# Optimization experiments

Hardware: AMD Instinct MI355X
Metric: run time of the kernel (lower is better)

## Reference

```python
import jax, jax.numpy as jnp
import numpy as np

EPS = 1e-5  # BatchNorm eps
K_NEIGH = 32


def cdist(a, b):
    # a: (B,M,3), b: (B,N,3) -> (B,M,N) euclidean distances
    d2 = (jnp.sum(a * a, -1)[:, :, None] + jnp.sum(b * b, -1)[:, None, :]
          - 2.0 * jnp.einsum('bmd,bnd->bmn', a, b))
    return jnp.sqrt(jnp.maximum(d2, 0.0))


def bn(x, axes):
    # training-mode BatchNorm with gamma=1, beta=0 (fresh init); channel = remaining axis
    m = jnp.mean(x, axes, keepdims=True)
    v = jnp.var(x, axes, keepdims=True)
    return (x - m) / jnp.sqrt(v + EPS)


def gather_nb(x, idx):
    # x: (B,N,C), idx: (B,M,k) int -> (B,M,k,C)
    return jax.vmap(lambda xb, ib: xb[ib])(x, idx)


def sa_wslfa(xyz, feat, M, k, Wf, bf, Wa, ba):
    # xyz: (B,N,3), feat: (B,N,C) channel-last
    B, N, _ = xyz.shape
    idxc = jnp.linspace(0.0, N - 1, M).astype(jnp.int32)  # fps_uniform
    centers = xyz[:, idxc]                                 # (B,M,3)
    d = cdist(centers, xyz)                                # (B,M,N)
    _, idx_knn = jax.lax.top_k(-d, min(k, N))              # k smallest dists
    nx = gather_nb(xyz, idx_knn) - centers[:, :, None, :]  # local coords (B,M,k,3)
    nf = gather_nb(feat, idx_knn)                          # (B,M,k,C)
    cat = jnp.concatenate([nx, nf], -1)                    # (B,M,k,3+C)
    fp = jax.nn.relu(bn(jnp.einsum('bmkd,od->bmko', cat, Wf) + bf, (0, 1, 2)))
    ain = jnp.concatenate([cat, fp - jnp.mean(fp, 2, keepdims=True)], -1)
    alpha = jax.nn.relu(bn(jnp.einsum('bmkd,od->bmko', ain, Wa) + ba, (0, 1, 2)))
    w = jax.nn.softmax(alpha, axis=2)                      # softmax over k neighbors
    return centers, jnp.sum(w * fp, axis=2)                # (B,M,out)


def fp_layer(xyz_l, xyz_h, fl, fh, W, b):
    # 3-NN inverse-distance interpolation + 1x1 conv MLP
    d = cdist(xyz_l, xyz_h)
    kk = min(3, xyz_h.shape[1])
    negd, idx = jax.lax.top_k(-d, kk)
    d3 = jnp.maximum(-negd, 1e-8)
    w = 1.0 / d3
    w = w / jnp.sum(w, -1, keepdims=True)
    fi = jnp.sum(w[..., None] * gather_nb(fh, idx), 2)     # (B,Nl,Ch)
    x = jnp.concatenate([fi, fl], -1)
    return jax.nn.relu(bn(jnp.einsum('bnc,oc->bno', x, W) + b, (0, 1)))


def _forward(X, W_spfe1, b_spfe1, W_spfe2, b_spfe2, Wf1, bf1, Wa1, ba1,
             Wf2, bf2, Wa2, ba2, Wf3, bf3, Wa3, ba3,
             Wfp3, bfp3, Wfp2, bfp2, Wfp1, bfp1, Wh1, bh1, Wh2, bh2):
    B, N, C = X.shape
    xyz = X[:, :, :3]
    xyz_c = xyz - jnp.mean(xyz, 1, keepdims=True)
    normals = jnp.zeros_like(xyz)                          # C==3 path: zero normals
    spfe_in = jnp.concatenate([xyz, xyz_c, normals], -1)   # (B,N,9)
    h = jax.nn.relu(bn(jnp.einsum('bnd,od->bno', spfe_in, W_spfe1) + b_spfe1, (0, 1)))
    f0 = jax.nn.relu(bn(jnp.einsum('bnd,od->bno', h, W_spfe2) + b_spfe2, (0, 1)))
    M1, M2, M3 = max(1, N // 4), max(1, N // 8), max(1, N // 16)
    xyz1, f1 = sa_wslfa(xyz, f0, M1, K_NEIGH, Wf1, bf1, Wa1, ba1)
    xyz2, f2 = sa_wslfa(xyz1, f1, M2, K_NEIGH, Wf2, bf2, Wa2, ba2)
    xyz3, f3 = sa_wslfa(xyz2, f2, M3, K_NEIGH, Wf3, bf3, Wa3, ba3)
    f_up2 = fp_layer(xyz2, xyz3, f2, f3, Wfp3, bfp3)
    f_up1 = fp_layer(xyz1, xyz2, f1, f_up2, Wfp2, bfp2)
    f_up0 = fp_layer(xyz, xyz1, f0, f_up1, Wfp1, bfp1)
    hh = jax.nn.relu(bn(jnp.einsum('bnc,oc->bno', f_up0, Wh1) + bh1, (0, 1)))
    # dropout is identity in deterministic reference
    return jnp.einsum('bnc,oc->bno', hh, Wh2) + bh2        # (B,N,num_classes)


def setup_inputs() -> dict:
    key = jax.random.key(0)
    ks = jax.random.split(key, 32)

    def w(i, o, c):
        return jax.random.normal(ks[i], (o, c), jnp.float32) * (2.0 / c) ** 0.5

    def bias(i, o):
        return jax.random.normal(ks[i], (o,), jnp.float32) * 0.01

    return {
        'X': jax.random.normal(ks[0], (8, 4096, 3), jnp.float32),
        'W_spfe1': w(1, 64, 9), 'b_spfe1': bias(2, 64),
        'W_spfe2': w(3, 64, 64), 'b_spfe2': bias(4, 64),
        'Wf1': w(5, 128, 67), 'bf1': bias(6, 128),
        'Wa1': w(7, 128, 195), 'ba1': bias(8, 128),
        'Wf2': w(9, 256, 131), 'bf2': bias(10, 256),
        'Wa2': w(11, 256, 387), 'ba2': bias(12, 256),
        'Wf3': w(13, 512, 259), 'bf3': bias(14, 512),
        'Wa3': w(15, 512, 771), 'ba3': bias(16, 512),
        'Wfp3': w(17, 256, 768), 'bfp3': bias(18, 256),
        'Wfp2': w(19, 128, 384), 'bfp2': bias(20, 128),
        'Wfp1': w(21, 128, 192), 'bfp1': bias(22, 128),
        'Wh1': w(23, 128, 128), 'bh1': bias(24, 128),
        'Wh2': w(25, 50, 128), 'bh2': bias(26, 50),
    }


def reference(X, W_spfe1, b_spfe1, W_spfe2, b_spfe2, Wf1, bf1, Wa1, ba1,
              Wf2, bf2, Wa2, ba2, Wf3, bf3, Wa3, ba3,
              Wfp3, bfp3, Wfp2, bfp2, Wfp1, bfp1, Wh1, bh1, Wh2, bh2):
    return _forward(X, W_spfe1, b_spfe1, W_spfe2, b_spfe2, Wf1, bf1, Wa1, ba1,
                    Wf2, bf2, Wa2, ba2, Wf3, bf3, Wa3, ba3,
                    Wfp3, bfp3, Wfp2, bfp2, Wfp1, bfp1, Wh1, bh1, Wh2, bh2)
```

## Files before the change

kernel.cpp:

```cpp
#include <hip/hip_runtime.h>
#include <hip/hip_bf16.h>
#include <cstdint>
#include <cstddef>

#define KN 32
#define EPSV 1e-5f
#define BR 64
#define BO 64
#define BKK 16
#define ASTR 68
#define BKM 32
#define BKP 40

typedef float f32x4 __attribute__((ext_vector_type(4)));
typedef __bf16 bf16x8 __attribute__((ext_vector_type(8)));
typedef unsigned short ushort8 __attribute__((ext_vector_type(8)));

static inline int ceil_div(int a, int b) { return (a + b - 1) / b; }

__device__ __forceinline__ float b2f(unsigned short u) {
  union { float f; uint32_t i; } x;
  x.i = (uint32_t)u << 16;
  return x.f;
}

__global__ void convw_kernel(const float* W, __hip_bfloat16* Wb, int wk, int colOff,
                             long long tot, int K) {
  long long i = (long long)blockIdx.x * blockDim.x + threadIdx.x;
  if (i >= tot) return;
  int o = (int)(i / K), c = (int)(i % K);
  Wb[i] = __float2bfloat16(W[(size_t)o * wk + colOff + c]);
}

struct MdArgs {
  const float* Af; const unsigned short* Ab; int lda;
  const float* W; int wk; int colOff;
  const unsigned short* Wb;
  float* outf; __hip_bfloat16* outb;
  float* partial; int numOt;
  const unsigned short* Ga; const float* Gm;
  const float* xyz; const float* ctr; const int* idx;
  int M, Ncur;
  int R, K, O;
};

template <int EP, bool ABF16, bool WBF16>
__global__ __launch_bounds__(256) void gemm_mdw(MdArgs g) {
  __shared__ __align__(16) char smemraw[(128 + 64) * BKP * 2];
  __shared__ float nxs[128][3];
  __shared__ float waxs[64][3];
  __shared__ int grow[128];
  __hip_bfloat16* As = (__hip_bfloat16*)smemraw;
  __hip_bfloat16* Ws = As + 128 * BKP;
  const int tid = threadIdx.x;
  const int lane = tid & 63, w = tid >> 6;
  const int cpx = gridDim.x >> 3;
  const int s = (blockIdx.x & 7) * cpx + (blockIdx.x >> 3);
  const int rt = s / g.numOt;
  const int ot = s - rt * g.numOt;
  const int br0 = rt * 128, bo0 = ot * BO;

  if constexpr (EP == 2) {
    if (tid < 128) {
      int r = br0 + tid;
      int bm = r >> 5;
      int b = bm / g.M;
      int n = g.idx[(size_t)bm * KN + (r & (KN - 1))];
      int nb = b * g.Ncur + n;
      grow[tid] = nb;
      nxs[tid][0] = g.xyz[(size_t)nb * 3 + 0] - g.ctr[(size_t)bm * 3 + 0];
      nxs[tid][1] = g.xyz[(size_t)nb * 3 + 1] - g.ctr[(size_t)bm * 3 + 1];
      nxs[tid][2] = g.xyz[(size_t)nb * 3 + 2] - g.ctr[(size_t)bm * 3 + 2];
    } else if (tid < 192) {
      int o = tid - 128;
      waxs[o][0] = g.W[(size_t)(bo0 + o) * g.wk + 0];
      waxs[o][1] = g.W[(size_t)(bo0 + o) * g.wk + 1];
      waxs[o][2] = g.W[(size_t)(bo0 + o) * g.wk + 2];
    }
  }

  f32x4 acc[2][4] = {};
  const int arow0 = (w * 16 + (lane & 15)) * BKP + (lane >> 4) * 8;
  const int arow1 = arow0 + 64 * BKP;
  const int wr = tid >> 2;
  const int wkb = (tid & 3) * 8;
  const float* wrow = WBF16 ? nullptr : (g.W + (size_t)(bo0 + wr) * g.wk + g.colOff);

  for (int k0 = 0; k0 < g.K; k0 += BKM) {
#pragma unroll
    for (int p = 0; p < 2; ++p) {
      int i = tid + p * 256;
      int r = i >> 2, c8 = (i & 3) * 8;
      if constexpr (ABF16) {
        ushort8 v = *(const ushort8*)(g.Ab + (size_t)(br0 + r) * g.lda + k0 + c8);
        *(ushort8*)((unsigned short*)As + r * BKP + c8) = v;
      } else {
        const float* ap = g.Af + (size_t)(br0 + r) * g.lda + k0 + c8;
#pragma unroll
        for (int e = 0; e < 8; ++e) As[r * BKP + c8 + e] = __float2bfloat16(ap[e]);
      }
    }
    if constexpr (WBF16) {
      ushort8 v = *(const ushort8*)(g.Wb + (size_t)(bo0 + wr) * g.K + k0 + wkb);
      *(ushort8*)((unsigned short*)Ws + wr * BKP + wkb) = v;
    } else {
#pragma unroll
      for (int e = 0; e < 8; ++e)
        Ws[wr * BKP + wkb + e] = __float2bfloat16(wrow[k0 + wkb + e]);
    }
    __syncthreads();
    bf16x8 av0 = *(const bf16x8*)(As + arow0);
    bf16x8 av1 = *(const bf16x8*)(As + arow1);
#pragma unroll
    for (int nf = 0; nf < 4; ++nf) {
      bf16x8 bv = *(const bf16x8*)(Ws + (nf * 16 + (lane & 15)) * BKP + (lane >> 4) * 8);
      acc[0][nf] = __builtin_amdgcn_mfma_f32_16x16x32_bf16(av0, bv, acc[0][nf], 0, 0, 0);
      acc[1][nf] = __builtin_amdgcn_mfma_f32_16x16x32_bf16(av1, bv, acc[1][nf], 0, 0, 0);
    }
    __syncthreads();
  }

  const int col0 = lane & 15;
  float* red0 = (float*)smemraw;
  float* red1 = (float*)smemraw + 256;

#pragma unroll
  for (int rf = 0; rf < 2; ++rf) {
    const int rbase = rf * 64 + w * 16 + (lane >> 4) * 4;
    if constexpr (EP == 0) {
#pragma unroll
      for (int nf = 0; nf < 4; ++nf) {
        int o = bo0 + nf * 16 + col0;
#pragma unroll
        for (int e = 0; e < 4; ++e)
          g.outf[(size_t)(br0 + rbase + e) * g.O + o] = acc[rf][nf][e];
      }
    }
    if constexpr (EP == 1) {
#pragma unroll
      for (int nf = 0; nf < 4; ++nf) {
        int o = bo0 + nf * 16 + col0;
#pragma unroll
        for (int e = 0; e < 4; ++e)
          g.outb[(size_t)(br0 + rbase + e) * g.O + o] = __float2bfloat16(acc[rf][nf][e]);
      }
    }
    if constexpr (EP == 2 || EP == 3) {
      float vals[4][4];
#pragma unroll
      for (int nf = 0; nf < 4; ++nf) {
        int ol = nf * 16 + col0;
        int o = bo0 + ol;
#pragma unroll
        for (int e = 0; e < 4; ++e) {
          int rl = rbase + e;
          float v = acc[rf][nf][e];
          if constexpr (EP == 2) {
            int bmg = (br0 + rl) >> 5;
            v += b2f(g.Ga[(size_t)grow[rl] * g.O + o]) +
                 nxs[rl][0] * waxs[ol][0] + nxs[rl][1] * waxs[ol][1] +
                 nxs[rl][2] * waxs[ol][2] - g.Gm[(size_t)bmg * g.O + o];
          }
          vals[nf][e] = v;
          if constexpr (EP == 2)
            g.outb[(size_t)(br0 + rl) * g.O + o] = __float2bfloat16(v);
          else
            g.outf[(size_t)(br0 + rl) * g.O + o] = v;
        }
      }
#pragma unroll
      for (int nf = 0; nf < 4; ++nf) {
        float s0 = vals[nf][0] + vals[nf][1] + vals[nf][2] + vals[nf][3];
        float s1 = vals[nf][0] * vals[nf][0] + vals[nf][1] * vals[nf][1] +
                   vals[nf][2] * vals[nf][2] + vals[nf][3] * vals[nf][3];
        s0 += __shfl_xor(s0, 16); s0 += __shfl_xor(s0, 32);
        s1 += __shfl_xor(s1, 16); s1 += __shfl_xor(s1, 32);
        if ((lane >> 4) == 0) {
          red0[w * 64 + nf * 16 + lane] = s0;
          red1[w * 64 + nf * 16 + lane] = s1;
        }
      }
      __syncthreads();
      if (tid < 64) {
        float t0 = red0[tid] + red0[64 + tid] + red0[128 + tid] + red0[192 + tid];
        float t1 = red1[tid] + red1[64 + tid] + red1[128 + tid] + red1[192 + tid];
        size_t base = ((size_t)(rt * 2 + rf) * g.numOt + ot) * 128;
        g.partial[base + tid] = t0;
        g.partial[base + 64 + tid] = t1;
      }
      __syncthreads();
    }
  }
}

__global__ __launch_bounds__(256) void combine_fp_kernel(
    const unsigned short* Gf, const float* Wf, int wk,
    const float* xyz, const float* ctr, const int* idx,
    __hip_bfloat16* fpout, float* partial, int numOt, int M, int Ncur, int O) {
  __shared__ float tile[64][68];
  __shared__ float nxs[64][3];
  __shared__ float wfx[64][3];
  __shared__ int grow[64];
  int tid = threadIdx.x;
  int rt = blockIdx.x, ot = blockIdx.y;
  int br0 = rt * 64, bo0 = ot * 64;
  if (tid < 64) {
    int r = br0 + tid;
    int bm = r >> 5;
    int b = bm / M;
    int n = idx[(size_t)bm * KN + (r & (KN - 1))];
    int nb = b * Ncur + n;
    grow[tid] = nb;
    nxs[tid][0] = xyz[(size_t)nb * 3 + 0] - ctr[(size_t)bm * 3 + 0];
    nxs[tid][1] = xyz[(size_t)nb * 3 + 1] - ctr[(size_t)bm * 3 + 1];
    nxs[tid][2] = xyz[(size_t)nb * 3 + 2] - ctr[(size_t)bm * 3 + 2];
  } else if (tid < 128) {
    int o = tid - 64;
    wfx[o][0] = Wf[(size_t)(bo0 + o) * wk + 0];
    wfx[o][1] = Wf[(size_t)(bo0 + o) * wk + 1];
    wfx[o][2] = Wf[(size_t)(bo0 + o) * wk + 2];
  }
  __syncthreads();
  int rr = tid >> 2, os = (tid & 3) * 16;
  const unsigned short* gr = Gf + (size_t)grow[rr] * O + bo0 + os;
  ushort8 v0 = *(const ushort8*)gr;
  ushort8 v1 = *(const ushort8*)(gr + 8);
  __hip_bfloat16* outp = fpout + (size_t)(br0 + rr) * O + bo0 + os;
  float nx0 = nxs[rr][0], nx1 = nxs[rr][1], nx2 = nxs[rr][2];
#pragma unroll
  for (int i = 0; i < 16; ++i) {
    float gv = b2f(i < 8 ? v0[i] : v1[i - 8]);
    int o = os + i;
    float val = gv + nx0 * wfx[o][0] + nx1 * wfx[o][1] + nx2 * wfx[o][2];
    tile[rr][o] = val;
    outp[i] = __float2bfloat16(val);
  }
  __syncthreads();
  if (tid < 64) {
    float s = 0.f, s2 = 0.f;
#pragma unroll 4
    for (int r2 = 0; r2 < 64; ++r2) {
      float v = tile[r2][tid];
      s += v; s2 += v * v;
    }
    size_t base = ((size_t)rt * numOt + ot) * 128;
    partial[base + tid] = s;
    partial[base + 64 + tid] = s2;
  }
}

__global__ __launch_bounds__(64) void bn_fpmean_kernel(__hip_bfloat16* fp, const float2* stats2,
                                                       __hip_bfloat16* outm, int O) {
  int bm = blockIdx.x;
  int o = blockIdx.y * 64 + threadIdx.x;
  float2 st = stats2[o];
  __hip_bfloat16* p = fp + (size_t)bm * KN * O + o;
  float s = 0.f;
#pragma unroll
  for (int kk = 0; kk < KN; ++kk) {
    float v = __bfloat162float(p[(size_t)kk * O]);
    float y = fmaxf((v - st.x) * st.y, 0.f);
    __hip_bfloat16 yb = __float2bfloat16(y);
    p[(size_t)kk * O] = yb;
    s += __bfloat162float(yb);
  }
  outm[(size_t)bm * O + o] = __float2bfloat16(s * (1.f / KN));
}

__global__ __launch_bounds__(64) void apply_lite_kernel(const __hip_bfloat16* alpha,
                                                        const __hip_bfloat16* fp,
                                                        const float2* stats2, float* fout, int O) {
  int bm = blockIdx.x;
  int o = blockIdx.y * 64 + threadIdx.x;
  float2 st = stats2[o];
  size_t base = (size_t)bm * KN * O + o;
  float a[KN];
  float mx = -3.4e38f;
#pragma unroll
  for (int kk = 0; kk < KN; ++kk) {
    float v = fmaxf((__bfloat162float(alpha[base + (size_t)kk * O]) - st.x) * st.y, 0.f);
    a[kk] = v; mx = fmaxf(mx, v);
  }
  float s = 0.f;
#pragma unroll
  for (int kk = 0; kk < KN; ++kk) { float e = expf(a[kk] - mx); a[kk] = e; s += e; }
  float acc = 0.f;
#pragma unroll
  for (int kk = 0; kk < KN; ++kk) acc += a[kk] * __bfloat162float(fp[base + (size_t)kk * O]);
  fout[(size_t)bm * O + o] = acc / s;
}

struct GemmArgs {
  const float* A; const float* W; const float* bias;
  float* out; __hip_bfloat16* outb;
  float* partial; const float2* stats2; float* fout;
  const __hip_bfloat16* fpb; const float* fpmean;
  const float* xyz; const float* feat; const float* ctr; const int* idx; const float* bmean;
  int R, K, O, numOt, M, Cf, Of, Ncur;
};

template <int EMODE, int MODE>
__global__ __launch_bounds__(256) void gemm_dense(GemmArgs g) {
  __shared__ float smem[2 * BKK * ASTR];
  float* As = smem;
  float* Ws = smem + BKK * ASTR;
  const int tid = threadIdx.x;
  const int tr = tid >> 4, tc = tid & 15;
  const int rt = blockIdx.x, ot = blockIdx.y;
  const int br0 = rt * BR, bo0 = ot * BO;
  float acc[4][4] = {};
  for (int k0 = 0; k0 < g.K; k0 += BKK) {
    for (int i = tid; i < BR * BKK; i += 256) {
      int rr = i >> 4, cc = i & 15;
      int c = k0 + cc;
      float v = 0.f;
      if (c < g.K) {
        if constexpr (MODE == 0) {
          v = g.A[(size_t)(br0 + rr) * g.K + c];
        } else {
          int r = br0 + rr;
          int b = r / g.Ncur, n = r - b * g.Ncur;
          if (c < 3) v = g.xyz[((size_t)b * g.Ncur + n) * 3 + c];
          else if (c < 6) v = g.xyz[((size_t)b * g.Ncur + n) * 3 + (c - 3)] - g.bmean[b * 3 + (c - 3)];
        }
      }
      As[cc * ASTR + rr] = v;
    }
    for (int i = tid; i < BO * BKK; i += 256) {
      int oo = i >> 4, cc = i & 15;
      int o = bo0 + oo, c = k0 + cc;
      Ws[cc * ASTR + oo] = (o < g.O && c < g.K) ? g.W[(size_t)o * g.K + c] : 0.f;
    }
    __syncthreads();
#pragma unroll
    for (int kk = 0; kk < BKK; ++kk) {
      float a0[4], w0[4];
#pragma unroll
      for (int i = 0; i < 4; ++i) a0[i] = As[kk * ASTR + tr * 4 + i];
#pragma unroll
      for (int j = 0; j < 4; ++j) w0[j] = Ws[kk * ASTR + tc * 4 + j];
#pragma unroll
      for (int i = 0; i < 4; ++i)
#pragma unroll
        for (int j = 0; j < 4; ++j) acc[i][j] += a0[i] * w0[j];
    }
    __syncthreads();
  }
#pragma unroll
  for (int i = 0; i < 4; ++i) {
    int r = br0 + tr * 4 + i;
    if (r >= g.R) continue;
#pragma unroll
    for (int j = 0; j < 4; ++j) {
      int o = bo0 + tc * 4 + j;
      if (o >= g.O) continue;
      float v = acc[i][j];
      if (EMODE == 0 && g.bias) v += g.bias[o];
      g.out[(size_t)r * g.O + o] = v;
    }
  }
  if constexpr (EMODE == 1) {
    float* red0 = smem;
    float* red1 = smem + 1024;
#pragma unroll
    for (int j = 0; j < 4; ++j) {
      float s0 = 0.f, s1 = 0.f;
#pragma unroll
      for (int i = 0; i < 4; ++i) { float v = acc[i][j]; s0 += v; s1 += v * v; }
      red0[tr * 64 + tc * 4 + j] = s0;
      red1[tr * 64 + tc * 4 + j] = s1;
    }
    __syncthreads();
    for (int st = 8; st >= 1; st >>= 1) {
      if (tr < st) {
#pragma unroll
        for (int j = 0; j < 4; ++j) {
          int cix = tc * 4 + j;
          red0[tr * 64 + cix] += red0[(tr + st) * 64 + cix];
          red1[tr * 64 + cix] += red1[(tr + st) * 64 + cix];
        }
      }
      __syncthreads();
    }
    if (tr == 0) {
      size_t base = ((size_t)rt * g.numOt + ot) * 128;
#pragma unroll
      for (int j = 0; j < 4; ++j) {
        int cix = tc * 4 + j;
        g.partial[base + cix] = red0[cix];
        g.partial[base + 64 + cix] = red1[cix];
      }
    }
  }
}

__global__ void reduce_finalize_kernel(const float* partial, float2* stats2,
                                       int Rt, int numOt, int R, int O) {
  int o = blockIdx.x;
  int ot = o >> 6, oo = o & 63;
  int tid = threadIdx.x;
  double s = 0.0, s2 = 0.0;
  for (int rtt = tid; rtt < Rt; rtt += 256) {
    const float* p = partial + ((size_t)rtt * numOt + ot) * 128;
    s += (double)p[oo];
    s2 += (double)p[64 + oo];
  }
  __shared__ double r0[256], r1[256];
  r0[tid] = s; r1[tid] = s2;
  __syncthreads();
  for (int st = 128; st > 0; st >>= 1) {
    if (tid < st) { r0[tid] += r0[tid + st]; r1[tid] += r1[tid + st]; }
    __syncthreads();
  }
  if (tid == 0) {
    double mu = r0[0] / R;
    double var = r1[0] / R - mu * mu;
    stats2[o] = make_float2((float)mu, 1.f / sqrtf((float)var + EPSV));
  }
}

template <bool BF16>
__global__ void bn_apply_relu_kernel(void* xv, const float2* stats2, long long tot, int C) {
  float* xf = (float*)xv;
  __hip_bfloat16* xb = (__hip_bfloat16*)xv;
  for (long long gidx = (long long)blockIdx.x * blockDim.x + threadIdx.x; gidx < tot;
       gidx += (long long)gridDim.x * blockDim.x) {
    int c = (int)(gidx % C);
    float2 st = stats2[c];
    float v = BF16 ? __bfloat162float(xb[gidx]) : xf[gidx];
    float y = fmaxf((v - st.x) * st.y, 0.f);
    if (BF16) xb[gidx] = __float2bfloat16(y);
    else xf[gidx] = y;
  }
}

__global__ void mean_xyz_kernel(const float* xyz, float* bmean, int N) {
  int b = blockIdx.x, tid = threadIdx.x;
  __shared__ float s[3][256];
  float sx = 0, sy = 0, sz = 0;
  for (int n = tid; n < N; n += 256) {
    const float* p = xyz + ((size_t)b * N + n) * 3;
    sx += p[0]; sy += p[1]; sz += p[2];
  }
  s[0][tid] = sx; s[1][tid] = sy; s[2][tid] = sz;
  __syncthreads();
  for (int st = 128; st > 0; st >>= 1) {
    if (tid < st) {
      s[0][tid] += s[0][tid + st];
      s[1][tid] += s[1][tid + st];
      s[2][tid] += s[2][tid + st];
    }
    __syncthreads();
  }
  if (tid < 3) bmean[b * 3 + tid] = s[tid][0] / (float)N;
}

__global__ void centers_kernel(const float* xyz, float* ctr, int B, int N, int M) {
  int g = blockIdx.x * blockDim.x + threadIdx.x;
  if (g >= B * M) return;
  int b = g / M, m = g % M;
  float delta = (float)(N - 1) / (float)(M - 1);
  int n = (int)((float)m * delta);
  if (n > N - 1) n = N - 1;
  ctr[(size_t)g * 3 + 0] = xyz[((size_t)b * N + n) * 3 + 0];
  ctr[(size_t)g * 3 + 1] = xyz[((size_t)b * N + n) * 3 + 1];
  ctr[(size_t)g * 3 + 2] = xyz[((size_t)b * N + n) * 3 + 2];
}

__global__ __launch_bounds__(1024) void knn_heads_kernel(const float* xyz, const float* ctr,
                                                         int* idx_out, int B, int N, int M) {
  extern __shared__ float sm[];
  const int pitch = N + (N >> 6);
  float* xs = sm;
  float* ys = sm + pitch;
  float* zs = sm + 2 * pitch;
  const int b = blockIdx.y;
  const int tid = threadIdx.x;
  const float* xb = xyz + (size_t)b * N * 3;
  for (int i = tid; i < N; i += blockDim.x) {
    int pi = i + (i >> 6);
    xs[pi] = xb[i * 3 + 0];
    ys[pi] = xb[i * 3 + 1];
    zs[pi] = xb[i * 3 + 2];
  }
  __syncthreads();
  const int w = tid >> 6, lane = tid & 63;
  const int wpb = blockDim.x >> 6;
  const int m = blockIdx.x * wpb + w;
  if (m >= M) return;
  const int bm = b * M + m;
  const float cx = ctr[(size_t)bm * 3], cy = ctr[(size_t)bm * 3 + 1], cz = ctr[(size_t)bm * 3 + 2];
  const float cc = cx * cx + cy * cy + cz * cz;
  const int npl = N >> 6;
  const int shift = 31 - __clz(npl);
  const int base = lane * npl;
  const int pb = base + (base >> 6);
  const float INF = 3.4e38f;
  const int IMAX = 0x7fffffff;

  float a0 = INF, a1 = INF, a2 = INF, a3 = INF;
  int i0 = IMAX, i1 = IMAX, i2 = IMAX, i3 = IMAX;
  for (int j = 0; j < npl; ++j) {
    float x = xs[pb + j], y = ys[pb + j], z = zs[pb + j];
    float d2 = cc + (x * x + y * y + z * z) - 2.f * (cx * x + cy * y + cz * z);
    int gj = base + j;
    bool lt0 = (d2 < a0) || (d2 == a0 && gj < i0);
    bool lt1 = (d2 < a1) || (d2 == a1 && gj < i1);
    bool lt2 = (d2 < a2) || (d2 == a2 && gj < i2);
    bool lt3 = (d2 < a3) || (d2 == a3 && gj < i3);
    float na3 = lt2 ? a2 : (lt3 ? d2 : a3); int ni3 = lt2 ? i2 : (lt3 ? gj : i3);
    float na2 = lt1 ? a1 : (lt2 ? d2 : a2); int ni2 = lt1 ? i1 : (lt2 ? gj : i2);
    float na1 = lt0 ? a0 : (lt1 ? d2 : a1); int ni1 = lt0 ? i0 : (lt1 ? gj : i1);
    float na0 = lt0 ? d2 : a0;              int ni0 = lt0 ? gj : i0;
    a0 = na0; a1 = na1; a2 = na2; a3 = na3;
    i0 = ni0; i1 = ni1; i2 = ni2; i3 = ni3;
  }

  unsigned int rmlo = 0u, rmhi = 0u;
  int remaining = npl;

  for (int sel = 0; sel < KN; ++sel) {
    float d = a0;
    int ii = i0;
#pragma unroll
    for (int off = 1; off < 64; off <<= 1) {
      float od = __shfl_xor(d, off);
      int oi = __shfl_xor(ii, off);
      if (od < d || (od == d && oi < ii)) { d = od; ii = oi; }
    }
    if (lane == 0) idx_out[(size_t)bm * KN + sel] = ii;
    const int owner = ii >> shift;
    if (lane == owner) {
      int jin = ii - (owner << shift);
      if (jin < 32) rmlo |= 1u << jin;
      else rmhi |= 1u << (jin - 32);
      remaining--;
      a0 = a1; i0 = i1; a1 = a2; i1 = i2; a2 = a3; i2 = i3;
      a3 = INF; i3 = IMAX;
    }
    if (sel == KN - 1) break;
    float h = __shfl(a0, owner);
    int remo = __shfl(remaining, owner);
    if (h >= INF && remo > 0) {
      unsigned int olo = __shfl(rmlo, owner);
      unsigned int ohi = __shfl(rmhi, owner);
      const int obase = owner << shift;
      const int opb = obase + (obase >> 6);
      float c0 = INF, c1 = INF, c2 = INF, c3 = INF;
      int jc0 = IMAX, jc1 = IMAX, jc2 = IMAX, jc3 = IMAX;
      if (lane < npl) {
        bool rem = (lane < 32) ? ((olo >> lane) & 1u) : ((ohi >> (lane - 32)) & 1u);
        if (!rem) {
          float x = xs[opb + lane], y = ys[opb + lane], z = zs[opb + lane];
          c0 = cc + (x * x + y * y + z * z) - 2.f * (cx * x + cy * y + cz * z);
          jc0 = obase + lane;
        }
      }
#pragma unroll
      for (int off = 1; off < 64; off <<= 1) {
        float b0v = __shfl_xor(c0, off), b1v = __shfl_xor(c1, off);
        float b2v = __shfl_xor(c2, off), b3v = __shfl_xor(c3, off);
        int d0v = __shfl_xor(jc0, off), d1v = __shfl_xor(jc1, off);
        int d2v = __shfl_xor(jc2, off), d3v = __shfl_xor(jc3, off);
        bool t1 = (c0 < b0v) || (c0 == b0v && jc0 < d0v);
        float o0 = t1 ? c0 : b0v; int p0 = t1 ? jc0 : d0v;
        float A0 = t1 ? c1 : c0, A1 = t1 ? c2 : c1, A2 = t1 ? c3 : c2;
        int IA0 = t1 ? jc1 : jc0, IA1 = t1 ? jc2 : jc1, IA2 = t1 ? jc3 : jc2;
        float B0 = t1 ? b0v : b1v, B1 = t1 ? b1v : b2v, B2 = t1 ? b2v : b3v;
        int IB0 = t1 ? d0v : d1v, IB1 = t1 ? d1v : d2v, IB2 = t1 ? d2v : d3v;
        bool t2 = (A0 < B0) || (A0 == B0 && IA0 < IB0);
        float o1 = t2 ? A0 : B0; int p1 = t2 ? IA0 : IB0;
        float A0b = t2 ? A1 : A0, A1b = t2 ? A2 : A1;
        int IA0b = t2 ? IA1 : IA0, IA1b = t2 ? IA2 : IA1;
        float B0b = t2 ? B0 : B1, B1b = t2 ? B1 : B2;
        int IB0b = t2 ? IB0 : IB1, IB1b = t2 ? IB1 : IB2;
        bool t3 = (A0b < B0b) || (A0b == B0b && IA0b < IB0b);
        float o2 = t3 ? A0b : B0b; int p2 = t3 ? IA0b : IB0b;
        float A0c = t3 ? A1b : A0b; int IA0c = t3 ? IA1b : IA0b;
        float B0c = t3 ? B0b : B1b; int IB0c = t3 ? IB0b : IB1b;
        bool t4 = (A0c < B0c) || (A0c == B0c && IA0c < IB0c);
        float o3 = t4 ? A0c : B0c; int p3 = t4 ? IA0c : IB0c;
        c0 = o0; c1 = o1; c2 = o2; c3 = o3;
        jc0 = p0; jc1 = p1; jc2 = p2; jc3 = p3;
      }
      if (lane == owner) {
        a0 = c0; a1 = c1; a2 = c2; a3 = c3;
        i0 = jc0; i1 = jc1; i2 = jc2; i3 = jc3;
      }
    }
  }
}

__global__ __launch_bounds__(256) void interp3_par_kernel(const float* xl, const float* xh,
                                                          int* idx3, float* w3, int Nl, int Nh) {
  extern __shared__ float sm[];
  float* xs = sm;
  float* ys = sm + Nh;
  float* zs = sm + 2 * Nh;
  const int b = blockIdx.y;
  const int tid = threadIdx.x;
  const float* xb = xh + (size_t)b * Nh * 3;
  for (int i = tid; i < Nh; i += 256) {
    xs[i] = xb[i * 3 + 0];
    ys[i] = xb[i * 3 + 1];
    zs[i] = xb[i * 3 + 2];
  }
  __syncthreads();
  const int pt = tid >> 2, sc = tid & 3;
  const int l = blockIdx.x * 64 + pt;
  if (l >= Nl) return;
  const size_t g = (size_t)b * Nl + l;
  const float px = xl[g * 3], py = xl[g * 3 + 1], pz = xl[g * 3 + 2];
  const float pp = px * px + py * py + pz * pz;
  const int chunk = Nh >> 2;
  const int j0 = sc * chunk, j1 = j0 + chunk;
  float a0 = 3.4e38f, a1 = 3.4e38f, a2 = 3.4e38f;
  int i0 = 0x7fffffff, i1 = 0x7fffffff, i2 = 0x7fffffff;
  for (int j = j0; j < j1; ++j) {
    float x = xs[j], y = ys[j], z = zs[j];
    float d2 = (pp + (x * x + y * y + z * z)) - 2.f * (px * x + py * y + pz * z);
    if (d2 < a0) {
      a2 = a1; i2 = i1; a1 = a0; i1 = i0; a0 = d2; i0 = j;
    } else if (d2 < a1) {
      a2 = a1; i2 = i1; a1 = d2; i1 = j;
    } else if (d2 < a2) {
      a2 = d2; i2 = j;
    }
  }
#pragma unroll
  for (int off = 1; off < 4; off <<= 1) {
    float b0 = __shfl_xor(a0, off), b1 = __shfl_xor(a1, off), b2 = __shfl_xor(a2, off);
    int c0 = __shfl_xor(i0, off), c1 = __shfl_xor(i1, off), c2 = __shfl_xor(i2, off);
    bool t = (a0 < b0) || (a0 == b0 && i0 < c0);
    float o0 = t ? a0 : b0; int oi0 = t ? i0 : c0;
    float na0 = t ? a1 : a0, na1 = t ? a2 : a1;
    int nia0 = t ? i1 : i0, nia1 = t ? i2 : i1;
    float nb0 = t ? b0 : b1, nb1 = t ? b1 : b2;
    int nib0 = t ? c0 : c1, nib1 = t ? c1 : c2;
    bool t2 = (na0 < nb0) || (na0 == nb0 && nia0 < nib0);
    float o1 = t2 ? na0 : nb0; int oi1 = t2 ? nia0 : nib0;
    float ma0 = t2 ? na1 : na0; int mia0 = t2 ? nia1 : nia0;
    float mb0 = t2 ? nb0 : nb1; int mib0 = t2 ? nib0 : nib1;
    bool t3 = (ma0 < mb0) || (ma0 == mb0 && mia0 < mib0);
    float o2 = t3 ? ma0 : mb0; int oi2 = t3 ? mia0 : mib0;
    a0 = o0; a1 = o1; a2 = o2; i0 = oi0; i1 = oi1; i2 = oi2;
  }
  if (sc == 0) {
    float d0 = fmaxf(sqrtf(fmaxf(a0, 0.f)), 1e-8f);
    float d1 = fmaxf(sqrtf(fmaxf(a1, 0.f)), 1e-8f);
    float d2_ = fmaxf(sqrtf(fmaxf(a2, 0.f)), 1e-8f);
    float w0 = 1.f / d0, w1 = 1.f / d1, w2 = 1.f / d2_;
    float s = w0 + w1 + w2;
    idx3[g * 3 + 0] = i0;
    idx3[g * 3 + 1] = i1;
    idx3[g * 3 + 2] = i2;
    w3[g * 3 + 0] = w0 / s;
    w3[g * 3 + 1] = w1 / s;
    w3[g * 3 + 2] = w2 / s;
  }
}

__global__ void buildx_kernel(const float* fh, const float* fl, const int* idx3, const float* w3,
                              float* xout, int B, int Nl, int Nh, int Ch, int Cl) {
  int Cx = Ch + Cl;
  size_t tot = (size_t)B * Nl * Cx;
  for (size_t g = (size_t)blockIdx.x * blockDim.x + threadIdx.x; g < tot;
       g += (size_t)gridDim.x * blockDim.x) {
    int r = (int)(g / Cx), c = (int)(g % Cx);
    int b = r / Nl;
    if (c < Ch) {
      float s = 0.f;
      for (int j = 0; j < 3; ++j) {
        int n = idx3[(size_t)r * 3 + j];
        s += w3[(size_t)r * 3 + j] * fh[((size_t)b * Nh + n) * Ch + c];
      }
      xout[g] = s;
    } else {
      xout[g] = fl[(size_t)r * Cl + (c - Ch)];
    }
  }
}

extern "C" void kernel_launch(void* const* d_in, const int* in_sizes, int n_in,
                              void* d_out, int out_size, void* d_ws, size_t ws_size,
                              hipStream_t stream) {
  const int B = 8, N = 4096;
  const float* X = (const float*)d_in[0];
  const float* W_spfe1 = (const float*)d_in[1];
  const float* W_spfe2 = (const float*)d_in[3];
  const float* Wf1 = (const float*)d_in[5];
  const float* Wa1 = (const float*)d_in[7];
  const float* Wf2 = (const float*)d_in[9];
  const float* Wa2 = (const float*)d_in[11];
  const float* Wf3 = (const float*)d_in[13];
  const float* Wa3 = (const float*)d_in[15];
  const float* Wfp3 = (const float*)d_in[17];
  const float* Wfp2 = (const float*)d_in[19];
  const float* Wfp1 = (const float*)d_in[21];
  const float* Wh1 = (const float*)d_in[23];
  const float* Wh2 = (const float*)d_in[25];
  const float* bh2 = (const float*)d_in[26];
  float* out = (float*)d_out;

  char* wp = (char*)d_ws;
  auto alloc = [&](size_t bytes) -> void* {
    void* p = (void*)wp;
    wp += (bytes + 255) & ~(size_t)255;
    return p;
  };
  float2* stats2 = (float2*)alloc(512 * sizeof(float2) * 2);
  float* partial = (float*)alloc((size_t)8192 * 128 * 4);
  float* bmean = (float*)alloc(B * 3 * sizeof(float));
  float* f0 = (float*)alloc((size_t)B * N * 64 * 4);
  float* xyz1 = (float*)alloc((size_t)B * 1024 * 3 * 4);
  float* xyz2 = (float*)alloc((size_t)B * 512 * 3 * 4);
  float* xyz3 = (float*)alloc((size_t)B * 256 * 3 * 4);
  float* f1 = (float*)alloc((size_t)B * 1024 * 128 * 4);
  float* f2 = (float*)alloc((size_t)B * 512 * 256 * 4);
  float* f3 = (float*)alloc((size_t)B * 256 * 512 * 4);
  float* fpmean = (float*)alloc((size_t)B * 1024 * 128 * 4);
  __hip_bfloat16* fpmeanb = (__hip_bfloat16*)alloc((size_t)B * 1024 * 128 * 2);
  int* idxb = (int*)alloc((size_t)B * 1024 * KN * 4);
  int* idx3 = (int*)alloc((size_t)B * 4096 * 3 * 4);
  float* w3 = (float*)alloc((size_t)B * 4096 * 3 * 4);
  void* BIG = alloc((size_t)33554432 * 2);
  size_t fup_off = (size_t)(wp - (char*)d_ws);
  float* fup2 = (float*)alloc((size_t)B * 512 * 256 * 4);
  float* fup1 = (float*)alloc((size_t)B * 1024 * 128 * 4);
  float* fup0 = (float*)alloc((size_t)B * 4096 * 128 * 4);
  __hip_bfloat16* alphaBuf_all = (__hip_bfloat16*)((char*)d_ws + fup_off);
  size_t alpha_end = fup_off + (size_t)67108864;
  char* wp2 = (char*)d_ws + alpha_end;
  if (wp2 < wp) wp2 = wp;
  __hip_bfloat16* Gfb = (__hip_bfloat16*)wp2; wp2 += (size_t)8 * 1024 * 1024;
  __hip_bfloat16* Gab = (__hip_bfloat16*)wp2; wp2 += (size_t)8 * 1024 * 1024;
  float* Gm = (float*)wp2; wp2 += (size_t)4 * 1024 * 1024;
  __hip_bfloat16* Wbuf = (__hip_bfloat16*)wp2; wp2 += (size_t)2 * 1024 * 1024;

  auto run_stats = [&](int R, int O) {
    reduce_finalize_kernel<<<O, 256, 0, stream>>>(partial, stats2, R / 64, O / 64, R, O);
  };
  auto run_bn = [&](void* x, int R, int C, bool bf) {
    long long tot = (long long)R * C;
    int blocks = (int)((tot + 255) / 256);
    if (blocks > 4096) blocks = 4096;
    if (bf) bn_apply_relu_kernel<true><<<blocks, 256, 0, stream>>>(x, stats2, tot, C);
    else bn_apply_relu_kernel<false><<<blocks, 256, 0, stream>>>(x, stats2, tot, C);
  };
  auto run_knn = [&](const float* xyz_in, const float* ctr, int Nc, int M) {
    int pitch = Nc + (Nc >> 6);
    size_t sm = (size_t)3 * pitch * 4;
    int wpb = (Nc >= 4096 && (M % 16) == 0) ? 16 : 4;
    knn_heads_kernel<<<dim3(M / wpb, B), wpb * 64, sm, stream>>>(xyz_in, ctr, idxb, B, Nc, M);
  };
  auto run_convw = [&](const float* W, int wk, int colOff, int O, int K) {
    long long tot = (long long)O * K;
    convw_kernel<<<(int)((tot + 255) / 256), 256, 0, stream>>>(W, Wbuf, wk, colOff, tot, K);
  };

  mean_xyz_kernel<<<B, 256, 0, stream>>>(X, bmean, N);
  float* hbuf = (float*)BIG;
  {
    GemmArgs g{};
    g.W = W_spfe1; g.out = hbuf; g.partial = partial;
    g.R = B * N; g.K = 9; g.O = 64; g.numOt = 1;
    g.xyz = X; g.bmean = bmean; g.Ncur = N;
    gemm_dense<1, 3><<<dim3(g.R / 64, 1), 256, 0, stream>>>(g);
    run_stats(g.R, g.O); run_bn(hbuf, g.R, g.O, false);
  }
  {
    GemmArgs g{};
    g.A = hbuf; g.W = W_spfe2; g.out = f0; g.partial = partial;
    g.R = B * N; g.K = 64; g.O = 64; g.numOt = 1;
    gemm_dense<1, 0><<<dim3(g.R / 64, 1), 256, 0, stream>>>(g);
    run_stats(g.R, g.O); run_bn(f0, g.R, g.O, false);
  }

  auto sa = [&](const float* xyz_in, const float* feat_in, int Nc, int M, int Cf, int Of,
                const float* Wf, const float* Wa, float* xyz_out, float* f_out) {
    int BM = B * M, R = BM * KN, NR = B * Nc;
    int wkF = 3 + Cf, wkA = 3 + Cf + Of;
    centers_kernel<<<ceil_div(BM, 256), 256, 0, stream>>>(xyz_in, xyz_out, B, Nc, M);
    run_knn(xyz_in, xyz_out, Nc, M);
    __hip_bfloat16* fpbuf = (__hip_bfloat16*)BIG;
    {
      run_convw(Wf, wkF, 3, Of, Cf);
      MdArgs m{}; m.Af = feat_in; m.lda = Cf; m.W = Wf; m.wk = wkF; m.colOff = 3;
      m.Wb = (const unsigned short*)Wbuf;
      m.R = NR; m.K = Cf; m.O = Of; m.outb = Gfb; m.numOt = Of / 64;
      gemm_mdw<1, false, true><<<dim3((Of / 64) * (NR / 128)), 256, 0, stream>>>(m);
    }
    combine_fp_kernel<<<dim3(R / 64, Of / 64), 256, 0, stream>>>(
        (const unsigned short*)Gfb, Wf, wkF, xyz_in, xyz_out, idxb, fpbuf,
        partial, Of / 64, M, Nc, Of);
    run_stats(R, Of);
    bn_fpmean_kernel<<<dim3(BM, Of / 64), 64, 0, stream>>>(fpbuf, stats2, fpmeanb, Of);
    {
      run_convw(Wa, wkA, 3, Of, Cf);
      MdArgs m{}; m.Af = feat_in; m.lda = Cf; m.W = Wa; m.wk = wkA; m.colOff = 3;
      m.Wb = (const unsigned short*)Wbuf;
      m.R = NR; m.K = Cf; m.O = Of; m.outb = Gab; m.numOt = Of / 64;
      gemm_mdw<1, false, true><<<dim3((Of / 64) * (NR / 128)), 256, 0, stream>>>(m);
    }
    run_convw(Wa, wkA, 3 + Cf, Of, Of);
    {
      MdArgs m{}; m.Ab = (const unsigned short*)fpmeanb; m.lda = Of; m.W = Wa; m.wk = wkA;
      m.colOff = 3 + Cf; m.Wb = (const unsigned short*)Wbuf;
      m.R = BM; m.K = Of; m.O = Of; m.outf = Gm; m.numOt = Of / 64;
      gemm_mdw<0, true, true><<<dim3((Of / 64) * (BM / 128)), 256, 0, stream>>>(m);
    }
    {
      MdArgs m{}; m.Ab = (const unsigned short*)fpbuf; m.lda = Of; m.W = Wa; m.wk = wkA;
      m.colOff = 3 + Cf; m.Wb = (const unsigned short*)Wbuf;
      m.R = R; m.K = Of; m.O = Of;
      m.outb = alphaBuf_all; m.partial = partial; m.numOt = Of / 64;
      m.Ga = (const unsigned short*)Gab; m.Gm = Gm;
      m.xyz = xyz_in; m.ctr = xyz_out; m.idx = idxb; m.M = M; m.Ncur = Nc;
      gemm_mdw<2, true, true><<<dim3((Of / 64) * (R / 128)), 256, 0, stream>>>(m);
    }
    run_stats(R, Of);
    apply_lite_kernel<<<dim3(BM, Of / 64), 64, 0, stream>>>(alphaBuf_all, fpbuf, stats2, f_out, Of);
  };

  sa(X, f0, 4096, 1024, 64, 128, Wf1, Wa1, xyz1, f1);
  sa(xyz1, f1, 1024, 512, 128, 256, Wf2, Wa2, xyz2, f2);
  sa(xyz2, f2, 512, 256, 256, 512, Wf3, Wa3, xyz3, f3);

  auto fpl = [&](const float* xl, const float* xh, const float* fl, const float* fh,
                 int Nl, int Nh, int Cl, int Ch, const float* W, float* f_up, int O) {
    size_t smI = (size_t)3 * Nh * 4;
    interp3_par_kernel<<<dim3(ceil_div(Nl, 64), B), 256, smI, stream>>>(xl, xh, idx3, w3, Nl, Nh);
    float* xbuf = (float*)BIG;
    int Cx = Ch + Cl;
    size_t tot = (size_t)B * Nl * Cx;
    int blocks = (int)((tot + 255) / 256);
    if (blocks > 4096) blocks = 4096;
    buildx_kernel<<<blocks, 256, 0, stream>>>(fh, fl, idx3, w3, xbuf, B, Nl, Nh, Ch, Cl);
    run_convw(W, Cx, 0, O, Cx);
    MdArgs m{};
    m.Af = xbuf; m.lda = Cx; m.W = W; m.wk = Cx; m.colOff = 0;
    m.R = B * Nl; m.K = Cx; m.O = O;
    m.Wb = (const unsigned short*)Wbuf;
    m.outf = f_up; m.partial = partial; m.numOt = O / 64;
    gemm_mdw<3, false, true><<<dim3((O / 64) * (m.R / 128)), 256, 0, stream>>>(m);
    run_stats(m.R, O); run_bn(f_up, m.R, O, false);
  };

  fpl(xyz2, xyz3, f2, f3, 512, 256, 256, 512, Wfp3, fup2, 256);
  fpl(xyz1, xyz2, f1, fup2, 1024, 512, 128, 256, Wfp2, fup1, 128);
  fpl(X, xyz1, f0, fup1, 4096, 1024, 64, 128, Wfp1, fup0, 128);

  float* hh = (float*)BIG;
  {
    run_convw(Wh1, 128, 0, 128, 128);
    MdArgs m{};
    m.Af = fup0; m.lda = 128; m.W = Wh1; m.wk = 128; m.colOff = 0;
    m.Wb = (const unsigned short*)Wbuf;
    m.R = B * N; m.K = 128; m.O = 128;
    m.outf = hh; m.partial = partial; m.numOt = 2;
    gemm_mdw<3, false, true><<<dim3(2 * (m.R / 128)), 256, 0, stream>>>(m);
    run_stats(m.R, m.O); run_bn(hh, m.R, m.O, false);
  }
  {
    GemmArgs g{};
    g.A = hh; g.W = Wh2; g.bias = bh2; g.out = out;
    g.R = B * N; g.K = 128; g.O = 50; g.numOt = 1;
    gemm_dense<0, 0><<<dim3(g.R / 64, 1), 256, 0, stream>>>(g);
  }
}
```

Before: 1.064 ms.

## Register-prefetch next GEMM K tile and merge Wf/Wa feature GEMMs

The MFMA GEMM kernel now loads the next K-slice of A and W into registers while the current tile is being multiplied, instead of loading and storing inside the same step. This hides global-memory latency at the cost of extra registers. Separately, the two per-point feature GEMMs (Wf and Wa columns applied to the same feat_in) are merged into one launch with doubled output width. The epilogue splits the output columns between two bf16 buffers, so feat_in is read once and one launch is saved.

```diff
diff --git a/kernel.cpp b/kernel.cpp
--- a/kernel.cpp
+++ b/kernel.cpp
@@ -24,6 +24,13 @@
   return x.f;
 }
 
+__device__ __forceinline__ unsigned short f2bu(float f) {
+  __hip_bfloat16 h = __float2bfloat16(f);
+  union { __hip_bfloat16 h; unsigned short u; } c;
+  c.h = h;
+  return c.u;
+}
+
 __global__ void convw_kernel(const float* W, __hip_bfloat16* Wb, int wk, int colOff,
                              long long tot, int K) {
   long long i = (long long)blockIdx.x * blockDim.x + threadIdx.x;
@@ -37,6 +44,7 @@
   const float* W; int wk; int colOff;
   const unsigned short* Wb;
   float* outf; __hip_bfloat16* outb;
+  __hip_bfloat16* outb2; int Oh;
   float* partial; int numOt;
   const unsigned short* Ga; const float* Gm;
   const float* xyz; const float* ctr; const int* idx;
@@ -82,33 +90,53 @@
   f32x4 acc[2][4] = {};
   const int arow0 = (w * 16 + (lane & 15)) * BKP + (lane >> 4) * 8;
   const int arow1 = arow0 + 64 * BKP;
+  const int sr = tid >> 2;
+  const int sc8 = (tid & 3) * 8;
   const int wr = tid >> 2;
   const int wkb = (tid & 3) * 8;
   const float* wrow = WBF16 ? nullptr : (g.W + (size_t)(bo0 + wr) * g.wk + g.colOff);
 
+  ushort8 rA0, rA1, rW;
+  if constexpr (ABF16) {
+    rA0 = *(const ushort8*)(g.Ab + (size_t)(br0 + sr) * g.lda + sc8);
+    rA1 = *(const ushort8*)(g.Ab + (size_t)(br0 + 64 + sr) * g.lda + sc8);
+  } else {
+    const float* ap0 = g.Af + (size_t)(br0 + sr) * g.lda + sc8;
+    const float* ap1 = g.Af + (size_t)(br0 + 64 + sr) * g.lda + sc8;
+#pragma unroll
+    for (int e = 0; e < 8; ++e) { rA0[e] = f2bu(ap0[e]); rA1[e] = f2bu(ap1[e]); }
+  }
+  if constexpr (WBF16) {
+    rW = *(const ushort8*)(g.Wb + (size_t)(bo0 + wr) * g.K + wkb);
+  } else {
+#pragma unroll
+    for (int e = 0; e < 8; ++e) rW[e] = f2bu(wrow[wkb + e]);
+  }
+
   for (int k0 = 0; k0 < g.K; k0 += BKM) {
-#pragma unroll
-    for (int p = 0; p < 2; ++p) {
-      int i = tid + p * 256;
-      int r = i >> 2, c8 = (i & 3) * 8;
+    *(ushort8*)((unsigned short*)As + sr * BKP + sc8) = rA0;
+    *(ushort8*)((unsigned short*)As + (64 + sr) * BKP + sc8) = rA1;
+    *(ushort8*)((unsigned short*)Ws + wr * BKP + wkb) = rW;
+    __syncthreads();
+    ushort8 nA0, nA1, nW;
+    const int k1 = k0 + BKM;
+    if (k1 < g.K) {
       if constexpr (ABF16) {
-        ushort8 v = *(const ushort8*)(g.Ab + (size_t)(br0 + r) * g.lda + k0 + c8);
-        *(ushort8*)((unsigned short*)As + r * BKP + c8) = v;
+        nA0 = *(const ushort8*)(g.Ab + (size_t)(br0 + sr) * g.lda + k1 + sc8);
+        nA1 = *(const ushort8*)(g.Ab + (size_t)(br0 + 64 + sr) * g.lda + k1 + sc8);
       } else {
-        const float* ap = g.Af + (size_t)(br0 + r) * g.lda + k0 + c8;
-#pragma unroll
-        for (int e = 0; e < 8; ++e) As[r * BKP + c8 + e] = __float2bfloat16(ap[e]);
-      }
-    }
-    if constexpr (WBF16) {
-      ushort8 v = *(const ushort8*)(g.Wb + (size_t)(bo0 + wr) * g.K + k0 + wkb);
-      *(ushort8*)((unsigned short*)Ws + wr * BKP + wkb) = v;
-    } else {
-#pragma unroll
-      for (int e = 0; e < 8; ++e)
-        Ws[wr * BKP + wkb + e] = __float2bfloat16(wrow[k0 + wkb + e]);
-    }
-    __syncthreads();
+        const float* ap0 = g.Af + (size_t)(br0 + sr) * g.lda + k1 + sc8;
+        const float* ap1 = g.Af + (size_t)(br0 + 64 + sr) * g.lda + k1 + sc8;
+#pragma unroll
+        for (int e = 0; e < 8; ++e) { nA0[e] = f2bu(ap0[e]); nA1[e] = f2bu(ap1[e]); }
+      }
+      if constexpr (WBF16) {
+        nW = *(const ushort8*)(g.Wb + (size_t)(bo0 + wr) * g.K + k1 + wkb);
+      } else {
+#pragma unroll
+        for (int e = 0; e < 8; ++e) nW[e] = f2bu(wrow[k1 + wkb + e]);
+      }
+    }
     bf16x8 av0 = *(const bf16x8*)(As + arow0);
     bf16x8 av1 = *(const bf16x8*)(As + arow1);
 #pragma unroll
@@ -118,6 +146,7 @@
       acc[1][nf] = __builtin_amdgcn_mfma_f32_16x16x32_bf16(av1, bv, acc[1][nf], 0, 0, 0);
     }
     __syncthreads();
+    rA0 = nA0; rA1 = nA1; rW = nW;
   }
 
   const int col0 = lane & 15;
@@ -140,9 +169,18 @@
 #pragma unroll
       for (int nf = 0; nf < 4; ++nf) {
         int o = bo0 + nf * 16 + col0;
+        __hip_bfloat16* dst;
+        int oc, ostr;
+        if (g.outb2) {
+          ostr = g.Oh;
+          if (o >= g.Oh) { dst = g.outb2; oc = o - g.Oh; }
+          else { dst = g.outb; oc = o; }
+        } else {
+          dst = g.outb; oc = o; ostr = g.O;
+        }
 #pragma unroll
         for (int e = 0; e < 4; ++e)
-          g.outb[(size_t)(br0 + rbase + e) * g.O + o] = __float2bfloat16(acc[rf][nf][e]);
+          dst[(size_t)(br0 + rbase + e) * ostr + oc] = __float2bfloat16(acc[rf][nf][e]);
       }
     }
     if constexpr (EP == 2 || EP == 3) {
@@ -753,9 +791,9 @@
     int wpb = (Nc >= 4096 && (M % 16) == 0) ? 16 : 4;
     knn_heads_kernel<<<dim3(M / wpb, B), wpb * 64, sm, stream>>>(xyz_in, ctr, idxb, B, Nc, M);
   };
-  auto run_convw = [&](const float* W, int wk, int colOff, int O, int K) {
+  auto run_convw = [&](const float* W, int wk, int colOff, int O, int K, __hip_bfloat16* dst) {
     long long tot = (long long)O * K;
-    convw_kernel<<<(int)((tot + 255) / 256), 256, 0, stream>>>(W, Wbuf, wk, colOff, tot, K);
+    convw_kernel<<<(int)((tot + 255) / 256), 256, 0, stream>>>(W, dst, wk, colOff, tot, K);
   };
 
   mean_xyz_kernel<<<B, 256, 0, stream>>>(X, bmean, N);
@@ -784,25 +822,20 @@
     run_knn(xyz_in, xyz_out, Nc, M);
     __hip_bfloat16* fpbuf = (__hip_bfloat16*)BIG;
     {
-      run_convw(Wf, wkF, 3, Of, Cf);
-      MdArgs m{}; m.Af = feat_in; m.lda = Cf; m.W = Wf; m.wk = wkF; m.colOff = 3;
+      run_convw(Wf, wkF, 3, Of, Cf, Wbuf);
+      run_convw(Wa, wkA, 3, Of, Cf, Wbuf + (size_t)Of * Cf);
+      MdArgs m{}; m.Af = feat_in; m.lda = Cf;
       m.Wb = (const unsigned short*)Wbuf;
-      m.R = NR; m.K = Cf; m.O = Of; m.outb = Gfb; m.numOt = Of / 64;
-      gemm_mdw<1, false, true><<<dim3((Of / 64) * (NR / 128)), 256, 0, stream>>>(m);
+      m.R = NR; m.K = Cf; m.O = 2 * Of; m.Oh = Of;
+      m.outb = Gfb; m.outb2 = Gab; m.numOt = (2 * Of) / 64;
+      gemm_mdw<1, false, true><<<dim3(((2 * Of) / 64) * (NR / 128)), 256, 0, stream>>>(m);
     }
     combine_fp_kernel<<<dim3(R / 64, Of / 64), 256, 0, stream>>>(
         (const unsigned short*)Gfb, Wf, wkF, xyz_in, xyz_out, idxb, fpbuf,
         partial, Of / 64, M, Nc, Of);
     run_stats(R, Of);
     bn_fpmean_kernel<<<dim3(BM, Of / 64), 64, 0, stream>>>(fpbuf, stats2, fpmeanb, Of);
-    {
-      run_convw(Wa, wkA, 3, Of, Cf);
-      MdArgs m{}; m.Af = feat_in; m.lda = Cf; m.W = Wa; m.wk = wkA; m.colOff = 3;
-      m.Wb = (const unsigned short*)Wbuf;
-      m.R = NR; m.K = Cf; m.O = Of; m.outb = Gab; m.numOt = Of / 64;
-      gemm_mdw<1, false, true><<<dim3((Of / 64) * (NR / 128)), 256, 0, stream>>>(m);
-    }
-    run_convw(Wa, wkA, 3 + Cf, Of, Of);
+    run_convw(Wa, wkA, 3 + Cf, Of, Of, Wbuf);
     {
       MdArgs m{}; m.Ab = (const unsigned short*)fpmeanb; m.lda = Of; m.W = Wa; m.wk = wkA;
       m.colOff = 3 + Cf; m.Wb = (const unsigned short*)Wbuf;
@@ -836,7 +869,7 @@
     int blocks = (int)((tot + 255) / 256);
     if (blocks > 4096) blocks = 4096;
     buildx_kernel<<<blocks, 256, 0, stream>>>(fh, fl, idx3, w3, xbuf, B, Nl, Nh, Ch, Cl);
-    run_convw(W, Cx, 0, O, Cx);
+    run_convw(W, Cx, 0, O, Cx, Wbuf);
     MdArgs m{};
     m.Af = xbuf; m.lda = Cx; m.W = W; m.wk = Cx; m.colOff = 0;
     m.R = B * Nl; m.K = Cx; m.O = O;
@@ -852,7 +885,7 @@
 
   float* hh = (float*)BIG;
   {
-    run_convw(Wh1, 128, 0, 128, 128);
+    run_convw(Wh1, 128, 0, 128, 128, Wbuf);
     MdArgs m{};
     m.Af = fup0; m.lda = 128; m.W = Wh1; m.wk = 128; m.colOff = 0;
     m.Wb = (const unsigned short*)Wbuf;
```

New measurement: 1.015 ms. 4.6% less time.
